# Performance work log

Hardware: AMD Instinct MI355X
Metric: run time of the kernel (lower is better)

## Reference

```python
import jax, jax.numpy as jnp
import numpy as np

N, F, H = 512, 256, 512

def _w(k, i, o):
    return jax.random.normal(k, (i, o), jnp.float32) * (1.0 / np.sqrt(i))

def setup_inputs() -> dict:
    key = jax.random.key(0)
    ks = jax.random.split(key, 12)
    z = lambda n: jnp.zeros((n,), jnp.float32)
    return {
        "node_features": jax.random.normal(ks[0], (N, F), jnp.float32),
        "adjacency": jax.random.uniform(ks[1], (N, N), jnp.float32),
        # GraphConv layers: neighbor linear (wl,bl) and self-loop (ws,bs)
        "gc1_wl": _w(ks[2], F, H), "gc1_bl": z(H), "gc1_ws": _w(ks[3], F, H), "gc1_bs": z(H),
        "gc2_wl": _w(ks[4], H, H), "gc2_bl": z(H), "gc2_ws": _w(ks[5], H, H), "gc2_bs": z(H),
        "gc3_wl": _w(ks[6], H, F), "gc3_bl": z(F), "gc3_ws": _w(ks[7], H, F), "gc3_bs": z(F),
        # edge MLP: Linear(2F,H) -> ReLU -> (dropout=identity, eval) -> Linear(H,H) -> ReLU -> Linear(H,1)
        "mlp_w1": _w(ks[8], 2 * F, H), "mlp_b1": z(H),
        "mlp_w2": _w(ks[9], H, H), "mlp_b2": z(H),
        "mlp_w3": _w(ks[10], H, 1), "mlp_b3": z(1),
    }

def _gconv(x, adj_norm, wl, bl, ws, bs):
    # adj_norm @ Linear(x) + SelfLoop(x)
    return adj_norm @ (x @ wl + bl) + (x @ ws + bs)

def reference(node_features, adjacency,
              gc1_wl, gc1_bl, gc1_ws, gc1_bs,
              gc2_wl, gc2_bl, gc2_ws, gc2_bs,
              gc3_wl, gc3_bl, gc3_ws, gc3_bs,
              mlp_w1, mlp_b1, mlp_w2, mlp_b2, mlp_w3, mlp_b3):
    # row-normalized adjacency (shared across all three layers)
    adj_norm = adjacency / (adjacency.sum(axis=1, keepdims=True) + 1e-8)
    x = jax.nn.relu(_gconv(node_features, adj_norm, gc1_wl, gc1_bl, gc1_ws, gc1_bs))
    x = jax.nn.relu(_gconv(x, adj_norm, gc2_wl, gc2_bl, gc2_ws, gc2_bs))
    emb = _gconv(x, adj_norm, gc3_wl, gc3_bl, gc3_ws, gc3_bs)  # [N, F]
    # vectorized all-pairs (i<j) edge scoring, symmetric scatter
    iu, ju = np.triu_indices(N, k=1)  # static index lists, P = N(N-1)/2
    ef = jnp.concatenate([emb[iu], emb[ju]], axis=-1)  # [P, 2F]
    h = jax.nn.relu(ef @ mlp_w1 + mlp_b1)
    h = jax.nn.relu(h @ mlp_w2 + mlp_b2)
    s = jax.nn.sigmoid((h @ mlp_w3 + mlp_b3)[:, 0])  # [P]
    edge_scores = jnp.zeros((N, N), emb.dtype).at[iu, ju].set(s).at[ju, iu].set(s)
    return emb, edge_scores
```

## Files before the change

### kernel.cpp

```cpp
#include <hip/hip_runtime.h>
#include <hip/hip_bf16.h>


#define NN 512
#define FF 256
#define HH 512

typedef __attribute__((ext_vector_type(8))) short s8v;
typedef __attribute__((ext_vector_type(4))) float f4v;

__device__ __forceinline__ ushort f2bf(float f) {
  unsigned u = __float_as_uint(f);
  unsigned r = (u + 0x7fffu + ((u >> 16) & 1u)) >> 16;
  return (ushort)r;
}

template <bool RELU>
__device__ __forceinline__ void gemm_tile64(
    int m0, int n0, int K,
    const float* __restrict__ A, int lda,
    const float* __restrict__ B, int ldb,
    const float* __restrict__ bias,
    const float* __restrict__ add, int ldadd,
    float* __restrict__ C, int ldc, int tid)
{
  __shared__ float As[64][18];
  __shared__ float Bs[64][68];
  float4 acc = {0.f, 0.f, 0.f, 0.f};
  const int ty = tid >> 4, tx = tid & 15;

  const int am = tid >> 4;
  const int ak = tid & 15;
  const int bk = tid >> 4;
  const int bn = tid & 15;

  float4 pa = *(const float4*)&A[(m0 + am) * lda + ak * 4];
  float4 pb0 = *(const float4*)&B[bk * ldb + n0 + bn * 4];
  float4 pb1 = *(const float4*)&B[(bk + 16) * ldb + n0 + bn * 4];
  float4 pb2 = *(const float4*)&B[(bk + 32) * ldb + n0 + bn * 4];
  float4 pb3 = *(const float4*)&B[(bk + 48) * ldb + n0 + bn * 4];

  for (int k0 = 0; k0 < K; k0 += 64) {
    As[ak * 4 + 0][am] = pa.x;
    As[ak * 4 + 1][am] = pa.y;
    As[ak * 4 + 2][am] = pa.z;
    As[ak * 4 + 3][am] = pa.w;
    *(float4*)&Bs[bk][bn * 4] = pb0;
    *(float4*)&Bs[bk + 16][bn * 4] = pb1;
    *(float4*)&Bs[bk + 32][bn * 4] = pb2;
    *(float4*)&Bs[bk + 48][bn * 4] = pb3;
    __syncthreads();
    if (k0 + 64 < K) {
      pa = *(const float4*)&A[(m0 + am) * lda + k0 + 64 + ak * 4];
      pb0 = *(const float4*)&B[(k0 + 64 + bk) * ldb + n0 + bn * 4];
      pb1 = *(const float4*)&B[(k0 + 80 + bk) * ldb + n0 + bn * 4];
      pb2 = *(const float4*)&B[(k0 + 96 + bk) * ldb + n0 + bn * 4];
      pb3 = *(const float4*)&B[(k0 + 112 + bk) * ldb + n0 + bn * 4];
    }
#pragma unroll
    for (int k = 0; k < 64; ++k) {
      float a = As[k][ty];
      float4 b = *(const float4*)&Bs[k][tx * 4];
      acc.x += a * b.x; acc.y += a * b.y; acc.z += a * b.z; acc.w += a * b.w;
    }
    __syncthreads();
  }

  int m = m0 + ty;
  float4 v = acc;
  if (bias) {
    float4 bv = *(const float4*)&bias[n0 + tx * 4];
    v.x += bv.x; v.y += bv.y; v.z += bv.z; v.w += bv.w;
  }
  if (add) {
    float4 d = *(const float4*)&add[m * ldadd + n0 + tx * 4];
    v.x += d.x; v.y += d.y; v.z += d.z; v.w += d.w;
  }
  if (RELU) {
    v.x = fmaxf(v.x, 0.f); v.y = fmaxf(v.y, 0.f);
    v.z = fmaxf(v.z, 0.f); v.w = fmaxf(v.w, 0.f);
  }
  *(float4*)&C[m * ldc + n0 + tx * 4] = v;
}

template <bool RELU>
__global__ __launch_bounds__(512)
void gemm_ks(int K,
             const float* __restrict__ A, int lda,
             const float* __restrict__ B0, const float* __restrict__ B1, int ldb,
             const float* __restrict__ bias0, const float* __restrict__ bias1,
             const float* __restrict__ add0, const float* __restrict__ add1, int ldadd,
             float* __restrict__ C0, float* __restrict__ C1, int ldc)
{
  const float* B = blockIdx.z ? B1 : B0;
  const float* bias = blockIdx.z ? bias1 : bias0;
  const float* add = blockIdx.z ? add1 : add0;
  float* C = blockIdx.z ? C1 : C0;
  const int n0 = blockIdx.x * 64;
  const int m0 = blockIdx.y * 16;
  const int tid = threadIdx.x;
  const int half = tid >> 8;
  const int t = tid & 255;
  const int ty = t >> 4, tx = t & 15;

  __shared__ float As[2][64][18];
  __shared__ float Bs[2][64][68];
  __shared__ float red[16][68];

  float4 acc = {0.f, 0.f, 0.f, 0.f};
  const int am = t >> 4, ak = t & 15;
  const int bk = t >> 4, bn = t & 15;
  const int Kh = K >> 1;
  const int kb = half * Kh;

  float4 pa = *(const float4*)&A[(m0 + am) * lda + kb + ak * 4];
  float4 pb0 = *(const float4*)&B[(kb + bk) * ldb + n0 + bn * 4];
  float4 pb1 = *(const float4*)&B[(kb + bk + 16) * ldb + n0 + bn * 4];
  float4 pb2 = *(const float4*)&B[(kb + bk + 32) * ldb + n0 + bn * 4];
  float4 pb3 = *(const float4*)&B[(kb + bk + 48) * ldb + n0 + bn * 4];

  for (int k0 = 0; k0 < Kh; k0 += 64) {
    As[half][ak * 4 + 0][am] = pa.x;
    As[half][ak * 4 + 1][am] = pa.y;
    As[half][ak * 4 + 2][am] = pa.z;
    As[half][ak * 4 + 3][am] = pa.w;
    *(float4*)&Bs[half][bk][bn * 4] = pb0;
    *(float4*)&Bs[half][bk + 16][bn * 4] = pb1;
    *(float4*)&Bs[half][bk + 32][bn * 4] = pb2;
    *(float4*)&Bs[half][bk + 48][bn * 4] = pb3;
    __syncthreads();
    if (k0 + 64 < Kh) {
      pa = *(const float4*)&A[(m0 + am) * lda + kb + k0 + 64 + ak * 4];
      pb0 = *(const float4*)&B[(kb + k0 + 64 + bk) * ldb + n0 + bn * 4];
      pb1 = *(const float4*)&B[(kb + k0 + 80 + bk) * ldb + n0 + bn * 4];
      pb2 = *(const float4*)&B[(kb + k0 + 96 + bk) * ldb + n0 + bn * 4];
      pb3 = *(const float4*)&B[(kb + k0 + 112 + bk) * ldb + n0 + bn * 4];
    }
#pragma unroll
    for (int k = 0; k < 64; ++k) {
      float a = As[half][k][ty];
      float4 b = *(const float4*)&Bs[half][k][tx * 4];
      acc.x += a * b.x; acc.y += a * b.y; acc.z += a * b.z; acc.w += a * b.w;
    }
    __syncthreads();
  }

  if (half) *(float4*)&red[ty][tx * 4] = acc;
  __syncthreads();
  if (!half) {
    float4 r = *(const float4*)&red[ty][tx * 4];
    float4 v = acc;
    v.x += r.x; v.y += r.y; v.z += r.z; v.w += r.w;
    int m = m0 + ty;
    if (bias) {
      float4 bv = *(const float4*)&bias[n0 + tx * 4];
      v.x += bv.x; v.y += bv.y; v.z += bv.z; v.w += bv.w;
    }
    if (add) {
      float4 d = *(const float4*)&add[m * ldadd + n0 + tx * 4];
      v.x += d.x; v.y += d.y; v.z += d.z; v.w += d.w;
    }
    if (RELU) {
      v.x = fmaxf(v.x, 0.f); v.y = fmaxf(v.y, 0.f);
      v.z = fmaxf(v.z, 0.f); v.w = fmaxf(v.w, 0.f);
    }
    *(float4*)&C[m * ldc + n0 + tx * 4] = v;
  }
}

template <bool RELU>
__global__ __launch_bounds__(1024)
void gemm_ks4(int K,
              const float* __restrict__ A, int lda,
              const float* __restrict__ B, int ldb,
              const float* __restrict__ add, int ldadd,
              float* __restrict__ C, int ldc)
{
  const int n0 = blockIdx.x * 64;
  const int m0 = blockIdx.y * 16;
  const int tid = threadIdx.x;
  const int q = tid >> 8;
  const int t = tid & 255;
  const int ty = t >> 4, tx = t & 15;

  __shared__ float As[4][64][18];
  __shared__ float Bs[4][64][68];
  __shared__ float red[3][16][68];

  float4 acc = {0.f, 0.f, 0.f, 0.f};
  const int am = ty, ak = tx;
  const int bk = ty, bn = tx;
  const int Kq = K >> 2;
  const int kb = q * Kq;

  float4 pa = *(const float4*)&A[(m0 + am) * lda + kb + ak * 4];
  float4 pb0 = *(const float4*)&B[(kb + bk) * ldb + n0 + bn * 4];
  float4 pb1 = *(const float4*)&B[(kb + bk + 16) * ldb + n0 + bn * 4];
  float4 pb2 = *(const float4*)&B[(kb + bk + 32) * ldb + n0 + bn * 4];
  float4 pb3 = *(const float4*)&B[(kb + bk + 48) * ldb + n0 + bn * 4];

  for (int k0 = 0; k0 < Kq; k0 += 64) {
    As[q][ak * 4 + 0][am] = pa.x;
    As[q][ak * 4 + 1][am] = pa.y;
    As[q][ak * 4 + 2][am] = pa.z;
    As[q][ak * 4 + 3][am] = pa.w;
    *(float4*)&Bs[q][bk][bn * 4] = pb0;
    *(float4*)&Bs[q][bk + 16][bn * 4] = pb1;
    *(float4*)&Bs[q][bk + 32][bn * 4] = pb2;
    *(float4*)&Bs[q][bk + 48][bn * 4] = pb3;
    __syncthreads();
    if (k0 + 64 < Kq) {
      pa = *(const float4*)&A[(m0 + am) * lda + kb + k0 + 64 + ak * 4];
      pb0 = *(const float4*)&B[(kb + k0 + 64 + bk) * ldb + n0 + bn * 4];
      pb1 = *(const float4*)&B[(kb + k0 + 80 + bk) * ldb + n0 + bn * 4];
      pb2 = *(const float4*)&B[(kb + k0 + 96 + bk) * ldb + n0 + bn * 4];
      pb3 = *(const float4*)&B[(kb + k0 + 112 + bk) * ldb + n0 + bn * 4];
    }
#pragma unroll
    for (int k = 0; k < 64; ++k) {
      float a = As[q][k][ty];
      float4 b = *(const float4*)&Bs[q][k][tx * 4];
      acc.x += a * b.x; acc.y += a * b.y; acc.z += a * b.z; acc.w += a * b.w;
    }
    __syncthreads();
  }

  if (q) *(float4*)&red[q - 1][ty][tx * 4] = acc;
  __syncthreads();
  if (!q) {
    float4 v = acc;
#pragma unroll
    for (int r = 0; r < 3; ++r) {
      float4 p = *(const float4*)&red[r][ty][tx * 4];
      v.x += p.x; v.y += p.y; v.z += p.z; v.w += p.w;
    }
    int m = m0 + ty;
    if (add) {
      float4 d = *(const float4*)&add[m * ldadd + n0 + tx * 4];
      v.x += d.x; v.y += d.y; v.z += d.z; v.w += d.w;
    }
    if (RELU) {
      v.x = fmaxf(v.x, 0.f); v.y = fmaxf(v.y, 0.f);
      v.z = fmaxf(v.z, 0.f); v.w = fmaxf(v.w, 0.f);
    }
    *(float4*)&C[m * ldc + n0 + tx * 4] = v;
  }
}

__global__ __launch_bounds__(256)
void prep_gemm1(const float* __restrict__ adj, float* __restrict__ adjn,
                const float* __restrict__ w2, ushort* __restrict__ w2t2,
                const float* __restrict__ node,
                const float* __restrict__ g1wl, const float* __restrict__ g1bl,
                const float* __restrict__ g1ws, const float* __restrict__ g1bs,
                float* __restrict__ Tb, float* __restrict__ Sb) {
  int b = blockIdx.x;
  int tid = threadIdx.x;
  if (b < 512) {
    int z = b >> 8, t = b & 255;
    int m0 = (t >> 3) * 16, n0 = (t & 7) * 64;
    gemm_tile64<false>(m0, n0, FF, node, FF, z ? g1ws : g1wl, HH,
                       z ? g1bs : g1bl, nullptr, 0, z ? Sb : Tb, HH, tid);
  } else if (b < 1024) {
    int row = b - 512;
    const float* r = adj + row * NN;
    float a0 = r[tid], a1 = r[tid + 256];
    float s = a0 + a1;
#pragma unroll
    for (int m = 1; m < 64; m <<= 1) s += __shfl_xor(s, m);
    __shared__ float wsum[4];
    if ((tid & 63) == 0) wsum[tid >> 6] = s;
    __syncthreads();
    float inv = 1.f / (wsum[0] + wsum[1] + wsum[2] + wsum[3] + 1e-8f);
    float* o = adjn + row * NN;
    o[tid] = a0 * inv;
    o[tid + 256] = a1 * inv;
  } else {
    int b2 = b - 1024;
    int slab = b2 >> 3;
    int col = (b2 & 7) * 64 + (tid >> 2);
    int kq = tid & 3;
    int k0 = slab * 32 + kq * 8;
    ushort tmp[8];
#pragma unroll
    for (int e = 0; e < 8; ++e) tmp[e] = f2bf(w2[(k0 + e) * HH + col]);
    ushort* dst = w2t2 + slab * 16384 + col * 32 + kq * 8;
    *(ushort4*)dst = *(ushort4*)tmp;
    *(ushort4*)(dst + 4) = *(ushort4*)&tmp[4];
  }
}

__global__ __launch_bounds__(512)
__attribute__((amdgpu_waves_per_eu(2, 2)))
void edge_mlp(const float* __restrict__ Amat, const float* __restrict__ Bmat,
              const ushort* __restrict__ w2t2,
              const float* __restrict__ b2, const float* __restrict__ w3,
              const float* __restrict__ b3,
              float* __restrict__ edges)
{
  __shared__ ushort h1s[2][128 * 128];
  __shared__ float rowsv[2][24][128];
  __shared__ float part[8][128];

  const int tb = (int)blockIdx.x;
  int bj = (int)((sqrtf(4.f * tb + 1.f) - 1.f) * 0.5f);
  while (bj * bj + bj > tb) --bj;
  while ((bj + 1) * (bj + 2) <= tb) ++bj;
  const int bi = tb - bj * bj - bj;

  const int tid = threadIdx.x;
  const int wid = tid >> 6;
  const int lane = tid & 63;
  const int l15 = lane & 15;
  const int lg = lane >> 4;

  const f4v zero = {0.f, 0.f, 0.f, 0.f};
  f4v acc[8][4];
#pragma unroll
  for (int mf = 0; mf < 8; ++mf)
#pragma unroll
    for (int nf = 0; nf < 4; ++nf) acc[mf][nf] = zero;

  const int r1 = tid >> 5, kc1 = tid & 31;
  const int r2 = 16 + (tid >> 5);
  const float* src1base = (r1 < 8) ? (Amat + (bi * 8 + r1) * HH)
                                   : (Bmat + (bj * 16 + r1 - 8) * HH);
  const float* src2base = Bmat + (bj * 16 + r2 - 8) * HH;

  float4 ra, rb;
  auto issue_rows = [&](int ch) {
    ra = *(const float4*)(src1base + ch * 128 + kc1 * 4);
    if (tid < 256) rb = *(const float4*)(src2base + ch * 128 + kc1 * 4);
  };
  auto write_rows = [&](int buf) {
    *(float4*)&rowsv[buf][r1][kc1 * 4] = ra;
    if (tid < 256) *(float4*)&rowsv[buf][r2][kc1 * 4] = rb;
  };
  auto build_h1 = [&](int buf) {
#pragma unroll
    for (int q = 0; q < 8; ++q) {
      int fidx = q * 512 + tid;
      int p = fidx >> 5;
      int k4 = fidx & 31;
      float4 av = *(const float4*)&rowsv[buf][p >> 4][k4 * 4];
      float4 bv = *(const float4*)&rowsv[buf][8 + (p & 15)][k4 * 4];
      ushort4 pk;
      pk.x = f2bf(fmaxf(av.x + bv.x, 0.f));
      pk.y = f2bf(fmaxf(av.y + bv.y, 0.f));
      pk.z = f2bf(fmaxf(av.z + bv.z, 0.f));
      pk.w = f2bf(fmaxf(av.w + bv.w, 0.f));
      int off = (p * 256 + k4 * 8) ^ ((p & 7) << 4);
      *(ushort4*)((char*)h1s[buf] + off) = pk;
    }
  };

  auto lgkm_barrier = [] {
    asm volatile("s_waitcnt lgkmcnt(0)" ::: "memory");
    __builtin_amdgcn_s_barrier();
  };

  issue_rows(0);
  write_rows(0);
  lgkm_barrier();
  build_h1(0);
  lgkm_barrier();

  const ushort* wbase = w2t2 + wid * 2048 + l15 * 32 + lg * 8;

  s8v nb0, nb1, nb2, nb3;
  nb0 = *(const s8v*)wbase;
  nb1 = *(const s8v*)(wbase + 512);
  nb2 = *(const s8v*)(wbase + 1024);
  nb3 = *(const s8v*)(wbase + 1536);

  auto slab_step = [&](int cur, int slab) {
    s8v cb0 = nb0, cb1 = nb1, cb2 = nb2, cb3 = nb3;
    if (slab < 15) {
      const ushort* wb = wbase + (slab + 1) * 16384;
      nb0 = *(const s8v*)wb;
      nb1 = *(const s8v*)(wb + 512);
      nb2 = *(const s8v*)(wb + 1024);
      nb3 = *(const s8v*)(wb + 1536);
    }
    int ks = slab & 3;
    __builtin_amdgcn_s_setprio(1);
#pragma unroll
    for (int mf = 0; mf < 8; ++mf) {
      int p = mf * 16 + l15;
      int off = (p * 256 + ks * 64 + lg * 16) ^ ((p & 7) << 4);
      s8v a = *(const s8v*)((const char*)h1s[cur] + off);
      acc[mf][0] = __builtin_amdgcn_mfma_f32_16x16x32_bf16(a, cb0, acc[mf][0], 0, 0, 0);
      acc[mf][1] = __builtin_amdgcn_mfma_f32_16x16x32_bf16(a, cb1, acc[mf][1], 0, 0, 0);
      acc[mf][2] = __builtin_amdgcn_mfma_f32_16x16x32_bf16(a, cb2, acc[mf][2], 0, 0, 0);
      acc[mf][3] = __builtin_amdgcn_mfma_f32_16x16x32_bf16(a, cb3, acc[mf][3], 0, 0, 0);
    }
    __builtin_amdgcn_s_setprio(0);
  };

#pragma unroll
  for (int ch = 0; ch < 4; ++ch) {
    int cur = ch & 1;
    if (ch < 3) issue_rows(ch + 1);
    slab_step(cur, ch * 4 + 0);
    slab_step(cur, ch * 4 + 1);
    if (ch < 3) write_rows(cur ^ 1);
    slab_step(cur, ch * 4 + 2);
    if (ch < 3) lgkm_barrier();
    slab_step(cur, ch * 4 + 3);
    if (ch < 3) {
      build_h1(cur ^ 1);
      lgkm_barrier();
    }
  }

  float bb[4], ww[4];
#pragma unroll
  for (int nf = 0; nf < 4; ++nf) {
    int col = wid * 64 + nf * 16 + l15;
    bb[nf] = b2[col];
    ww[nf] = w3[col];
  }
#pragma unroll
  for (int mf = 0; mf < 8; ++mf) {
    float ps[4];
#pragma unroll
    for (int e = 0; e < 4; ++e) {
      ps[e] = fmaxf(acc[mf][0][e] + bb[0], 0.f) * ww[0] +
              fmaxf(acc[mf][1][e] + bb[1], 0.f) * ww[1] +
              fmaxf(acc[mf][2][e] + bb[2], 0.f) * ww[2] +
              fmaxf(acc[mf][3][e] + bb[3], 0.f) * ww[3];
    }
#pragma unroll
    for (int m = 1; m < 16; m <<= 1) {
#pragma unroll
      for (int e = 0; e < 4; ++e) ps[e] += __shfl_xor(ps[e], m);
    }
    if (l15 == 0) {
#pragma unroll
      for (int e = 0; e < 4; ++e)
        part[wid][mf * 16 + lg * 4 + e] = ps[e];
    }
  }
  __syncthreads();
  if (tid < 128) {
    float tot = b3[0];
#pragma unroll
    for (int w = 0; w < 8; ++w) tot += part[w][tid];
    float sg = 1.f / (1.f + expf(-tot));
    int i = bi * 8 + (tid >> 4);
    int j = bj * 16 + (tid & 15);
    if (i < j) {
      edges[i * NN + j] = sg;
      edges[j * NN + i] = sg;
    } else if (i == j) {
      edges[i * NN + i] = 0.f;
    }
  }
}

extern "C" void kernel_launch(void* const* d_in, const int* in_sizes, int n_in,
                              void* d_out, int out_size, void* d_ws, size_t ws_size,
                              hipStream_t stream) {
  const float* node = (const float*)d_in[0];
  const float* adj  = (const float*)d_in[1];
  const float* g1wl = (const float*)d_in[2];
  const float* g1bl = (const float*)d_in[3];
  const float* g1ws = (const float*)d_in[4];
  const float* g1bs = (const float*)d_in[5];
  const float* g2wl = (const float*)d_in[6];
  const float* g2bl = (const float*)d_in[7];
  const float* g2ws = (const float*)d_in[8];
  const float* g2bs = (const float*)d_in[9];
  const float* g3wl = (const float*)d_in[10];
  const float* g3bl = (const float*)d_in[11];
  const float* g3ws = (const float*)d_in[12];
  const float* g3bs = (const float*)d_in[13];
  const float* w1 = (const float*)d_in[14];
  const float* b1 = (const float*)d_in[15];
  const float* w2 = (const float*)d_in[16];
  const float* b2 = (const float*)d_in[17];
  const float* w3 = (const float*)d_in[18];
  const float* b3 = (const float*)d_in[19];

  float* out = (float*)d_out;
  float* emb = out;
  float* edges = out + NN * FF;

  char* wsb = (char*)d_ws;
  float* adjn = (float*)wsb;
  float* Tb   = (float*)(wsb + (1u << 20));
  float* Sb   = (float*)(wsb + (2u << 20));
  float* xa   = (float*)(wsb + (3u << 20));
  float* xb   = (float*)(wsb + (4u << 20));
  ushort* w2t2 = (ushort*)(wsb + (5u << 20));
  float* Amat = Tb;
  float* Bmat = Sb;

  prep_gemm1<<<1152, 256, 0, stream>>>(adj, adjn, w2, w2t2, node,
                                       g1wl, g1bl, g1ws, g1bs, Tb, Sb);
  gemm_ks4<true><<<dim3(8, 32), 1024, 0, stream>>>(
      NN, adjn, NN, Tb, HH, Sb, HH, xa, HH);
  gemm_ks<false><<<dim3(8, 32, 2), 512, 0, stream>>>(
      HH, xa, HH, g2wl, g2ws, HH, g2bl, g2bs,
      nullptr, nullptr, 0, Tb, Sb, HH);
  gemm_ks4<true><<<dim3(8, 32), 1024, 0, stream>>>(
      NN, adjn, NN, Tb, HH, Sb, HH, xb, HH);
  gemm_ks<false><<<dim3(4, 32, 2), 512, 0, stream>>>(
      HH, xb, HH, g3wl, g3ws, FF, g3bl, g3bs,
      nullptr, nullptr, 0, Tb, Sb, FF);
  gemm_ks<false><<<dim3(4, 32, 1), 512, 0, stream>>>(
      NN, adjn, NN, Tb, Tb, FF, nullptr, nullptr,
      Sb, Sb, FF, emb, emb, FF);
  gemm_ks<false><<<dim3(8, 32, 2), 512, 0, stream>>>(
      FF, emb, FF, w1, w1 + FF * HH, HH, b1, nullptr,
      nullptr, nullptr, 0, Amat, Bmat, HH);

  edge_mlp<<<1056, 512, 0, stream>>>(Amat, Bmat, w2t2, b2, w3, b3, edges);
}
```

Before: 168.1 us.

## Generalize 4-way split-K GEMM to dual outputs, stagger edge MLP h1 build

Result: slower. 341.0 us (+102.8%).

```diff
diff --git a/kernel.cpp b/kernel.cpp
--- a/kernel.cpp
+++ b/kernel.cpp
@@ -10,9 +10,9 @@
 typedef __attribute__((ext_vector_type(4))) float f4v;
 
 __device__ __forceinline__ ushort f2bf(float f) {
-  unsigned u = __float_as_uint(f);
-  unsigned r = (u + 0x7fffu + ((u >> 16) & 1u)) >> 16;
-  return (ushort)r;
+  union { __hip_bfloat16 h; ushort u; } b;
+  b.h = __float2bfloat16(f);
+  return b.u;
 }
 
 template <bool RELU>
@@ -172,10 +172,15 @@
 __global__ __launch_bounds__(1024)
 void gemm_ks4(int K,
               const float* __restrict__ A, int lda,
-              const float* __restrict__ B, int ldb,
-              const float* __restrict__ add, int ldadd,
-              float* __restrict__ C, int ldc)
+              const float* __restrict__ B0, const float* __restrict__ B1, int ldb,
+              const float* __restrict__ bias0, const float* __restrict__ bias1,
+              const float* __restrict__ add0, const float* __restrict__ add1, int ldadd,
+              float* __restrict__ C0, float* __restrict__ C1, int ldc)
 {
+  const float* B = blockIdx.z ? B1 : B0;
+  const float* bias = blockIdx.z ? bias1 : bias0;
+  const float* add = blockIdx.z ? add1 : add0;
+  float* C = blockIdx.z ? C1 : C0;
   const int n0 = blockIdx.x * 64;
   const int m0 = blockIdx.y * 16;
   const int tid = threadIdx.x;
@@ -235,6 +240,10 @@
       v.x += p.x; v.y += p.y; v.z += p.z; v.w += p.w;
     }
     int m = m0 + ty;
+    if (bias) {
+      float4 bv = *(const float4*)&bias[n0 + tx * 4];
+      v.x += bv.x; v.y += bv.y; v.z += bv.z; v.w += bv.w;
+    }
     if (add) {
       float4 d = *(const float4*)&add[m * ldadd + n0 + tx * 4];
       v.x += d.x; v.y += d.y; v.z += d.z; v.w += d.w;
@@ -405,11 +414,18 @@
     slab_step(cur, ch * 4 + 1);
     if (ch < 3) write_rows(cur ^ 1);
     slab_step(cur, ch * 4 + 2);
-    if (ch < 3) lgkm_barrier();
-    slab_step(cur, ch * 4 + 3);
     if (ch < 3) {
-      build_h1(cur ^ 1);
       lgkm_barrier();
+      if (wid & 1) {
+        slab_step(cur, ch * 4 + 3);
+        build_h1(cur ^ 1);
+      } else {
+        build_h1(cur ^ 1);
+        slab_step(cur, ch * 4 + 3);
+      }
+      lgkm_barrier();
+    } else {
+      slab_step(cur, ch * 4 + 3);
     }
   }
 
@@ -498,17 +514,19 @@
 
   prep_gemm1<<<1152, 256, 0, stream>>>(adj, adjn, w2, w2t2, node,
                                        g1wl, g1bl, g1ws, g1bs, Tb, Sb);
-  gemm_ks4<true><<<dim3(8, 32), 1024, 0, stream>>>(
-      NN, adjn, NN, Tb, HH, Sb, HH, xa, HH);
+  gemm_ks4<true><<<dim3(8, 32, 1), 1024, 0, stream>>>(
+      NN, adjn, NN, Tb, Tb, HH, nullptr, nullptr,
+      Sb, Sb, HH, xa, xa, HH);
   gemm_ks<false><<<dim3(8, 32, 2), 512, 0, stream>>>(
       HH, xa, HH, g2wl, g2ws, HH, g2bl, g2bs,
       nullptr, nullptr, 0, Tb, Sb, HH);
-  gemm_ks4<true><<<dim3(8, 32), 1024, 0, stream>>>(
-      NN, adjn, NN, Tb, HH, Sb, HH, xb, HH);
-  gemm_ks<false><<<dim3(4, 32, 2), 512, 0, stream>>>(
+  gemm_ks4<true><<<dim3(8, 32, 1), 1024, 0, stream>>>(
+      NN, adjn, NN, Tb, Tb, HH, nullptr, nullptr,
+      Sb, Sb, HH, xb, xb, HH);
+  gemm_ks4<false><<<dim3(4, 32, 2), 1024, 0, stream>>>(
       HH, xb, HH, g3wl, g3ws, FF, g3bl, g3bs,
       nullptr, nullptr, 0, Tb, Sb, FF);
-  gemm_ks<false><<<dim3(4, 32, 1), 512, 0, stream>>>(
+  gemm_ks4<false><<<dim3(4, 32, 1), 1024, 0, stream>>>(
       NN, adjn, NN, Tb, Tb, FF, nullptr, nullptr,
       Sb, Sb, FF, emb, emb, FF);
   gemm_ks<false><<<dim3(8, 32, 2), 512, 0, stream>>>(
```
